# Performance work log

Measured on AMD Instinct MI355X. Metric: run time of the kernel, lower is better.

The kernel has to match this reference:

```python
import jax, jax.numpy as jnp
import numpy as np
import math

THETA = 10000.0

def apply_rope(x, start_pos=0):
    # x: [B, H, S, D], rotate-half RoPE
    B, H, S, D = x.shape
    pos = jnp.arange(start_pos, start_pos + S, dtype=jnp.float32)
    inv_freq = 1.0 / (THETA ** (jnp.arange(0, D, 2, dtype=jnp.float32) / D))  # [D/2]
    ang = pos[:, None] * inv_freq[None, :]  # [S, D/2]
    cos, sin = jnp.cos(ang), jnp.sin(ang)
    x1, x2 = jnp.split(x, 2, axis=-1)
    return jnp.concatenate([x1 * cos - x2 * sin, x1 * sin + x2 * cos], axis=-1)


def setup_inputs() -> dict:
    key = jax.random.key(0)
    ks = jax.random.split(key, 9)
    B, S, E, H, D = 2, 2048, 2048, 16, 128
    s = 0.02
    return {
        "x": jax.random.normal(ks[0], (B, S, E), jnp.float32),
        "W_q": jax.random.normal(ks[1], (E, H * D), jnp.float32) * s,
        "b_q": jnp.zeros((H * D,), jnp.float32),
        "W_k": jax.random.normal(ks[2], (E, D), jnp.float32) * s,
        "b_k": jnp.zeros((D,), jnp.float32),
        "W_v": jax.random.normal(ks[3], (E, D), jnp.float32) * s,
        "b_v": jnp.zeros((D,), jnp.float32),
        "W_o": jax.random.normal(ks[4], (H * D, E), jnp.float32) * s,
        "b_o": jnp.zeros((E,), jnp.float32),
    }


def reference(x, W_q, b_q, W_k, b_k, W_v, b_v, W_o, b_o):
    B, S, E = x.shape
    D = W_k.shape[1]
    H = W_q.shape[1] // D
    # projections (weights stored [in, out])
    q = (x @ W_q + b_q).reshape(B, S, H, D).transpose(0, 2, 1, 3)   # [B,H,S,D]
    k = (x @ W_k + b_k).reshape(B, S, 1, D).transpose(0, 2, 1, 3)   # [B,1,S,D]
    v = (x @ W_v + b_v).reshape(B, S, 1, D).transpose(0, 2, 1, 3)   # [B,1,S,D]
    # RoPE (cache is None -> start_pos = 0)
    q = apply_rope(q, 0)
    k = apply_rope(k, 0)
    # shared-KV attention: k head dim broadcasts over H q heads
    scores = jnp.einsum("bhqd,bokd->bhqk", q, k) / math.sqrt(D)     # [B,H,S,S]
    causal = jnp.tril(jnp.ones((S, S), dtype=bool))
    scores = jnp.where(causal, scores, -jnp.inf)
    attn = jax.nn.softmax(scores, axis=-1)
    out = jnp.einsum("bhqk,bokd->bhqd", attn, v)                    # [B,H,S,D]
    out = out.transpose(0, 2, 1, 3).reshape(B, S, H * D)
    out = out @ W_o + b_o                                           # dropout is identity in eval
    return out
```

## Files before the change

### kernel.cpp

```cpp
#include <hip/hip_runtime.h>
#include <stdint.h>

typedef __bf16 bf16x8 __attribute__((ext_vector_type(8)));
typedef __bf16 bf16x2 __attribute__((ext_vector_type(2)));
typedef float  f32x4  __attribute__((ext_vector_type(4)));
typedef short  s16x8  __attribute__((ext_vector_type(8)));

__device__ inline unsigned short f2b(float f) {
  unsigned int u = __builtin_bit_cast(unsigned int, f);
  u += 0x7FFFu + ((u >> 16) & 1u);
  return (unsigned short)(u >> 16);
}
__device__ inline float b2f(unsigned short h) {
  unsigned int u = ((unsigned int)h) << 16;
  return __builtin_bit_cast(float, u);
}
__device__ inline unsigned int pkcvt(float a, float b) {
  bf16x2 t;
  t[0] = (__bf16)a;
  t[1] = (__bf16)b;
  return __builtin_bit_cast(unsigned int, t);
}
__device__ inline void gload_lds16(const void* g, void* l) {
  __builtin_amdgcn_global_load_lds(
      (const __attribute__((address_space(1))) unsigned int*)g,
      (__attribute__((address_space(3))) unsigned int*)l, 16, 0, 0);
}

__global__ void k_cvt_bf16(const float* __restrict__ in, unsigned short* __restrict__ out, int n4) {
  int i = blockIdx.x * blockDim.x + threadIdx.x;
  if (i < n4) {
    float4 v = ((const float4*)in)[i];
    ushort4 o;
    o.x = f2b(v.x); o.y = f2b(v.y); o.z = f2b(v.z); o.w = f2b(v.w);
    ((ushort4*)out)[i] = o;
  }
}

__global__ void k_transpose(const float* __restrict__ Wq, const float* __restrict__ Wk,
                            const float* __restrict__ Wv, const float* __restrict__ Wo,
                            unsigned short* __restrict__ dstQKV, unsigned short* __restrict__ dstO) {
  __shared__ float tile[32][33];
  int n0 = blockIdx.x * 32;
  int k0 = blockIdx.y * 32;
  const float* src; int ldn, noff, K;
  unsigned short* dst;
  if (blockIdx.z == 0) {
    K = 2048; dst = dstQKV;
    if (n0 < 2048)       { src = Wq; ldn = 2048; noff = n0; }
    else if (n0 < 2176)  { src = Wk; ldn = 128;  noff = n0 - 2048; }
    else                 { src = Wv; ldn = 128;  noff = n0 - 2176; }
  } else {
    if (n0 >= 2048) return;
    K = 2048; dst = dstO;
    src = Wo; ldn = 2048; noff = n0;
  }
  int tx = threadIdx.x & 31, ty = threadIdx.x >> 5;
  for (int yy = ty; yy < 32; yy += 8)
    tile[yy][tx] = src[(size_t)(k0 + yy) * ldn + noff + tx];
  __syncthreads();
  for (int yy = ty; yy < 32; yy += 8)
    dst[(size_t)(n0 + yy) * K + k0 + tx] = f2b(tile[tx][yy]);
}

template<int BIAS3>
__global__ __launch_bounds__(256)
void k_gemm96(const unsigned short* __restrict__ A, const unsigned short* __restrict__ Bt,
              const float* __restrict__ b0, const float* __restrict__ b1,
              const float* __restrict__ b2, unsigned short* __restrict__ Cout,
              int M, int N, int K) {
  __shared__ unsigned short As[3][4096];
  __shared__ unsigned short Bs[3][3072];
  const int tid  = threadIdx.x;
  const int lane = tid & 63, wid = tid >> 6;
  const int lr = lane & 15, lk = lane >> 4;
  const int wr = wid >> 1,  wc = wid & 1;

  const int nwg = gridDim.x * gridDim.y;
  const int flat = blockIdx.y * gridDim.x + blockIdx.x;
  const int swz = (flat & 7) * (nwg >> 3) + (flat >> 3);
  const int mb = (swz / gridDim.x) * 128;
  const int nb = (swz % gridDim.x) * 96;

  const int srow = tid >> 2, scb = (tid & 3) * 8;
  const size_t gA = (size_t)(mb + srow) * K + scb;
  const int brow0 = wid * 32 + (lane >> 2);
  const int bcol  = (lane & 3) * 8;
  const size_t gB = (size_t)(nb + brow0) * K + bcol;
  const int bdst0 = (wid * 128 + lane) * 16;

  f32x4 acc[4][3];
  #pragma unroll
  for (int i = 0; i < 4; ++i)
    #pragma unroll
    for (int j = 0; j < 3; ++j) acc[i][j] = (f32x4){0.f, 0.f, 0.f, 0.f};

  auto stage = [&](int buf, int kt) {
    const size_t ko = (size_t)kt * 32;
    gload_lds16(A + gA + ko,                  &As[buf][(tid) * 8]);
    gload_lds16(A + gA + 64 * (size_t)K + ko, &As[buf][2048 + tid * 8]);
    if (wid < 3) {
      gload_lds16(Bt + gB + ko,                  (char*)&Bs[buf][0] + bdst0);
      gload_lds16(Bt + gB + 16 * (size_t)K + ko, (char*)&Bs[buf][0] + bdst0 + 1024);
    }
  };

  const int ktn = K >> 5;
  stage(0, 0);
  stage(1, 1);

  int cur = 0;
  #pragma unroll 1
  for (int kt = 0; kt < ktn; ++kt) {
    if (kt + 2 < ktn) {
      int nbuf = cur + 2; if (nbuf >= 3) nbuf -= 3;
      stage(nbuf, kt + 2);
      if (wid < 3) asm volatile("s_waitcnt vmcnt(8)" ::: "memory");
      else         asm volatile("s_waitcnt vmcnt(4)" ::: "memory");
    } else if (kt + 1 < ktn) {
      if (wid < 3) asm volatile("s_waitcnt vmcnt(4)" ::: "memory");
      else         asm volatile("s_waitcnt vmcnt(2)" ::: "memory");
    } else {
      asm volatile("s_waitcnt vmcnt(0)" ::: "memory");
    }
    __builtin_amdgcn_sched_barrier(0);
    __builtin_amdgcn_s_barrier();
    bf16x8 af[4], bfv[3];
    #pragma unroll
    for (int m = 0; m < 4; ++m)
      af[m]  = *(const bf16x8*)&As[cur][(wr * 64 + m * 16 + lr) * 32 + lk * 8];
    #pragma unroll
    for (int n = 0; n < 3; ++n)
      bfv[n] = *(const bf16x8*)&Bs[cur][(wc * 48 + n * 16 + lr) * 32 + lk * 8];
    #pragma unroll
    for (int m = 0; m < 4; ++m)
      #pragma unroll
      for (int n = 0; n < 3; ++n)
        acc[m][n] = __builtin_amdgcn_mfma_f32_16x16x32_bf16(af[m], bfv[n], acc[m][n], 0, 0, 0);
    __builtin_amdgcn_s_barrier();
    ++cur; if (cur == 3) cur = 0;
  }

  const int r0 = mb + wr * 64, c0 = nb + wc * 48;
  #pragma unroll
  for (int m = 0; m < 4; ++m) {
    #pragma unroll
    for (int n = 0; n < 3; ++n) {
      int col = c0 + n * 16 + lr;
      float bb;
      if (BIAS3) bb = (col < 2048) ? b0[col] : (col < 2176 ? b1[col - 2048] : b2[col - 2176]);
      else       bb = b0[col];
      #pragma unroll
      for (int r = 0; r < 4; ++r) {
        int row = r0 + m * 16 + lk * 4 + r;
        Cout[(size_t)row * N + col] = f2b(acc[m][n][r] + bb);
      }
    }
  }
}

template<int OUT_BF16, int BIAS3>
__global__ __launch_bounds__(256)
void k_gemm_lds(const unsigned short* __restrict__ A, const unsigned short* __restrict__ Bt,
                const float* __restrict__ b0, const float* __restrict__ b1,
                const float* __restrict__ b2, void* __restrict__ Cout,
                int M, int N, int K) {
  __shared__ unsigned short As[3][4096];
  __shared__ unsigned short Bs[3][4096];
  const int tid  = threadIdx.x;
  const int lane = tid & 63, wid = tid >> 6;
  const int lr = lane & 15, lk = lane >> 4;
  const int wr = wid >> 1,  wc = wid & 1;

  const int nwg = gridDim.x * gridDim.y;
  const int flat = blockIdx.y * gridDim.x + blockIdx.x;
  const int swz = (flat & 7) * (nwg >> 3) + (flat >> 3);
  const int mb = (swz / gridDim.x) * 128;
  const int nb = (swz % gridDim.x) * 128;

  const int srow = tid >> 2, scb = (tid & 3) * 8;
  const size_t gA = (size_t)(mb + srow) * K + scb;
  const size_t gB = (size_t)(nb + srow) * K + scb;
  const int ldso = wid * 512;

  f32x4 acc[4][4];
  #pragma unroll
  for (int i = 0; i < 4; ++i)
    #pragma unroll
    for (int j = 0; j < 4; ++j) acc[i][j] = (f32x4){0.f, 0.f, 0.f, 0.f};

  auto stage = [&](int buf, int kt) {
    const size_t ko = (size_t)kt * 32;
    gload_lds16(A  + gA + ko,                  &As[buf][ldso]);
    gload_lds16(A  + gA + 64 * (size_t)K + ko, &As[buf][2048 + ldso]);
    gload_lds16(Bt + gB + ko,                  &Bs[buf][ldso]);
    gload_lds16(Bt + gB + 64 * (size_t)K + ko, &Bs[buf][2048 + ldso]);
  };

  const int ktn = K >> 5;
  stage(0, 0);
  stage(1, 1);

  int cur = 0;
  #pragma unroll 1
  for (int kt = 0; kt < ktn; ++kt) {
    if (kt + 2 < ktn) {
      int nbuf = cur + 2; if (nbuf >= 3) nbuf -= 3;
      stage(nbuf, kt + 2);
      asm volatile("s_waitcnt vmcnt(8)" ::: "memory");
    } else if (kt + 1 < ktn) {
      asm volatile("s_waitcnt vmcnt(4)" ::: "memory");
    } else {
      asm volatile("s_waitcnt vmcnt(0)" ::: "memory");
    }
    __builtin_amdgcn_sched_barrier(0);
    __builtin_amdgcn_s_barrier();
    bf16x8 af[4], bfv[4];
    #pragma unroll
    for (int m = 0; m < 4; ++m)
      af[m]  = *(const bf16x8*)&As[cur][(wr * 64 + m * 16 + lr) * 32 + lk * 8];
    #pragma unroll
    for (int n = 0; n < 4; ++n)
      bfv[n] = *(const bf16x8*)&Bs[cur][(wc * 64 + n * 16 + lr) * 32 + lk * 8];
    #pragma unroll
    for (int m = 0; m < 4; ++m)
      #pragma unroll
      for (int n = 0; n < 4; ++n)
        acc[m][n] = __builtin_amdgcn_mfma_f32_16x16x32_bf16(af[m], bfv[n], acc[m][n], 0, 0, 0);
    __builtin_amdgcn_s_barrier();
    ++cur; if (cur == 3) cur = 0;
  }

  const int r0 = mb + wr * 64, c0 = nb + wc * 64;
  #pragma unroll
  for (int m = 0; m < 4; ++m) {
    #pragma unroll
    for (int n = 0; n < 4; ++n) {
      int col = c0 + n * 16 + lr;
      float bb;
      if (BIAS3) bb = (col < 2048) ? b0[col] : (col < 2176 ? b1[col - 2048] : b2[col - 2176]);
      else       bb = b0[col];
      #pragma unroll
      for (int r = 0; r < 4; ++r) {
        int row = r0 + m * 16 + lk * 4 + r;
        float v = acc[m][n][r] + bb;
        if (OUT_BF16) ((unsigned short*)Cout)[(size_t)row * N + col] = f2b(v);
        else          ((float*)Cout)[(size_t)row * N + col] = v;
      }
    }
  }
}

__global__ void k_rope(const unsigned short* __restrict__ qkv,
                       unsigned short* __restrict__ qr,
                       unsigned short* __restrict__ kr,
                       int S, int H) {
  int R = blockIdx.x * 4 + (threadIdx.x >> 6);
  int lane = threadIdx.x & 63;
  int per_b = S * (H + 1);
  int b = R / per_b;
  int rem = R - b * per_b;
  int s = rem / (H + 1);
  int j = rem - s * (H + 1);
  const unsigned short* src = qkv + (size_t)(b * S + s) * 2304 + (j < H ? j * 128 : 2048);
  float x1 = b2f(src[lane]);
  float x2 = b2f(src[lane + 64]);
  float invf = expf(-(float)lane * (9.210340371976184f / 64.0f));
  float ang = (float)s * invf;
  float c = cosf(ang), sn = sinf(ang);
  float o1 = x1 * c - x2 * sn;
  float o2 = x1 * sn + x2 * c;
  unsigned short* dst;
  if (j < H) {
    const float scale = 0.08838834764831845f;
    o1 *= scale; o2 *= scale;
    dst = qr + ((size_t)(b * H + j) * S + s) * 128;
  } else {
    dst = kr + ((size_t)(b * S) + s) * 128;
  }
  dst[lane]      = f2b(o1);
  dst[lane + 64] = f2b(o2);
}

__global__ void k_vtrans(const unsigned short* __restrict__ qkv,
                         unsigned short* __restrict__ vt, int S) {
  __shared__ unsigned short tile[32][33];
  int b = blockIdx.z;
  int s0 = blockIdx.x * 32, d0 = blockIdx.y * 32;
  int tx = threadIdx.x & 31, ty = threadIdx.x >> 5;
  for (int yy = ty; yy < 32; yy += 8)
    tile[yy][tx] = qkv[(size_t)(b * S + s0 + yy) * 2304 + 2176 + d0 + tx];
  __syncthreads();
  for (int yy = ty; yy < 32; yy += 8)
    vt[((size_t)b * 128 + d0 + yy) * S + s0 + tx] = tile[tx][yy];
}

__global__ __launch_bounds__(256, 2)
void k_attn(const unsigned short* __restrict__ qr,
            const unsigned short* __restrict__ kr,
            const unsigned short* __restrict__ vt,
            unsigned short* __restrict__ attn_out,
            unsigned short* __restrict__ pscr,
            float* __restrict__ lscr,
            int S, int H) {
  const int flat = blockIdx.x + 16 * blockIdx.y + 256 * blockIdx.z;
  const int half = flat >> 8;
  const int p    = flat & 7;
  const int h    = (flat >> 3) & 15;
  const int b    = (flat >> 7) & 1;
  const int qtA = 8 + p, qtB = 7 - p;
  const int qb0A = qtA * 128, qb0B = qtB * 128;
  const int nA = 2 * qtA + 2;
  const int pg = (b * H + h) * 8 + p;

  const int tid = threadIdx.x, wid = tid >> 6, lane = tid & 63;
  const int lr = lane & 15, lk = lane >> 4;

  __shared__ unsigned short Kt[2][64 * 128];
  __shared__ unsigned short Vt[2][128 * 64];

  const char* kbyte = (const char*)(kr + (size_t)b * S * 128);
  const char* vbyte = (const char*)(vt + (size_t)b * 128 * S);
  const size_t vrow_bytes = (size_t)S * 2;

  bf16x8 aq[2][4];
  auto loadQ = [&](int qb0) {
    #pragma unroll
    for (int g = 0; g < 2; ++g) {
      const unsigned short* qptr = qr + ((size_t)(b * H + h) * S + (qb0 + wid * 32 + g * 16 + lr)) * 128;
      #pragma unroll
      for (int kk = 0; kk < 4; ++kk) aq[g][kk] = *(const bf16x8*)(qptr + kk * 32 + lk * 8);
    }
  };

  f32x4 acc[2][8];
  float ls[2];
  auto resetAcc = [&]() {
    #pragma unroll
    for (int g = 0; g < 2; ++g) {
      ls[g] = 0.f;
      #pragma unroll
      for (int t = 0; t < 8; ++t) acc[g][t] = (f32x4){0.f, 0.f, 0.f, 0.f};
    }
  };

  const int vsw = ((lr & 3) | ((lr >> 1) & 4)) << 4;
  int krow_[4], ksw_[4];
  #pragma unroll
  for (int m = 0; m < 4; ++m) {
    int row = ((m >> 1) << 5) + ((m & 1) << 2) + ((lr >> 2) << 3) + (lr & 3);
    krow_[m] = row;
    ksw_[m] = ((row & 3) | ((row >> 1) & 4)) << 4;
  }

  auto stage = [&](int buf, int kb) {
    const char* kg = kbyte + (size_t)kb * 256;
    #pragma unroll
    for (int r = 0; r < 4; ++r) {
      int row = (tid >> 4) + r * 16;
      int sw = ((row & 3) | ((row >> 1) & 4)) << 4;
      const char* src = kg + row * 256 + (((tid & 15) << 4) ^ sw);
      gload_lds16(src, (void*)((char*)&Kt[buf][0] + r * 4096 + wid * 1024));
    }
    const char* vg = vbyte + (size_t)kb * 2;
    #pragma unroll
    for (int r = 0; r < 4; ++r) {
      int d = (tid >> 3) + r * 32;
      int sw = ((d & 3) | ((d >> 1) & 4)) << 4;
      const char* src = vg + (size_t)d * vrow_bytes + (((tid & 7) << 4) ^ sw);
      gload_lds16(src, (void*)((char*)&Vt[buf][0] + r * 4096 + wid * 1024));
    }
  };

  auto itemKb = [&](int j, int& which) -> int {
    int idx = half * 17 + j;
    if (idx < nA) { which = 0; return idx * 64; }
    which = 1; return (idx - nA) * 64;
  };

  auto flushA = [&]() {
    #pragma unroll
    for (int g = 0; g < 2; ++g) {
      float v = ls[g];
      v += __shfl_xor(v, 16);
      v += __shfl_xor(v, 32);
      if (lk == 0) lscr[((size_t)pg * 2 + half) * 128 + wid * 32 + g * 16 + lr] = v;
      #pragma unroll
      for (int t = 0; t < 8; ++t)
        #pragma unroll
        for (int r = 0; r < 4; ++r) {
          int row = wid * 32 + g * 16 + lk * 4 + r;
          pscr[((size_t)pg * 2 + half) * 16384 + row * 128 + t * 16 + lr] = f2b(acc[g][t][r]);
        }
    }
  };

  auto computeTile = [&](int cur, int kb, int qb0cur) {
    const int qw = qb0cur + wid * 32;
    if (kb > qw + 31) return;
    const unsigned short* Kc = &Kt[cur][0];
    const unsigned short* Vc = &Vt[cur][0];
    f32x4 s4[2][4];
    #pragma unroll
    for (int g = 0; g < 2; ++g)
      #pragma unroll
      for (int m = 0; m < 4; ++m) s4[g][m] = (f32x4){0.f, 0.f, 0.f, 0.f};
    __builtin_amdgcn_s_setprio(1);
    #pragma unroll
    for (int kk = 0; kk < 4; ++kk) {
      bf16x8 kfk[4];
      #pragma unroll
      for (int m = 0; m < 4; ++m)
        kfk[m] = *(const bf16x8*)((const char*)Kc + krow_[m] * 256 + ((kk * 64 + lk * 16) ^ ksw_[m]));
      #pragma unroll
      for (int m = 0; m < 4; ++m) {
        s4[0][m] = __builtin_amdgcn_mfma_f32_16x16x32_bf16(kfk[m], aq[0][kk], s4[0][m], 0, 0, 0);
        s4[1][m] = __builtin_amdgcn_mfma_f32_16x16x32_bf16(kfk[m], aq[1][kk], s4[1][m], 0, 0, 0);
      }
    }
    __builtin_amdgcn_s_setprio(0);
    bf16x8 pa[2][2];
    #pragma unroll
    for (int g = 0; g < 2; ++g) {
      const int rowq = qw + g * 16 + lr;
      const bool domask = (kb + 64) > (qw + g * 16);
      uint2 pk[4];
      #pragma unroll
      for (int m = 0; m < 4; ++m) {
        const int kb_m = kb + ((m >> 1) << 5) + ((m & 1) << 2) + lk * 8;
        float pv[4];
        #pragma unroll
        for (int r = 0; r < 4; ++r) {
          float v = __expf(s4[g][m][r]);
          if (domask && (kb_m + r) > rowq) v = 0.f;
          pv[r] = v;
          ls[g] += v;
        }
        pk[m].x = pkcvt(pv[0], pv[1]);
        pk[m].y = pkcvt(pv[2], pv[3]);
      }
      uint4 ua, ub;
      ua.x = pk[0].x; ua.y = pk[0].y; ua.z = pk[1].x; ua.w = pk[1].y;
      ub.x = pk[2].x; ub.y = pk[2].y; ub.z = pk[3].x; ub.w = pk[3].y;
      pa[g][0] = __builtin_bit_cast(bf16x8, ua);
      pa[g][1] = __builtin_bit_cast(bf16x8, ub);
    }
    __builtin_amdgcn_s_setprio(1);
    #pragma unroll
    for (int t = 0; t < 8; ++t) {
      const char* vl = (const char*)(Vc + (t * 16 + lr) * 64);
      bf16x8 bv0 = *(const bf16x8*)(vl + ((lk * 16) ^ vsw));
      bf16x8 bv1 = *(const bf16x8*)(vl + ((64 + lk * 16) ^ vsw));
      acc[0][t] = __builtin_amdgcn_mfma_f32_16x16x32_bf16(pa[0][0], bv0, acc[0][t], 0, 0, 0);
      acc[1][t] = __builtin_amdgcn_mfma_f32_16x16x32_bf16(pa[1][0], bv0, acc[1][t], 0, 0, 0);
      acc[0][t] = __builtin_amdgcn_mfma_f32_16x16x32_bf16(pa[0][1], bv1, acc[0][t], 0, 0, 0);
      acc[1][t] = __builtin_amdgcn_mfma_f32_16x16x32_bf16(pa[1][1], bv1, acc[1][t], 0, 0, 0);
    }
    __builtin_amdgcn_s_setprio(0);
  };

  loadQ(qb0A);
  resetAcc();
  int curTile = 0, qb0cur = qb0A;

  {
    int wh0;
    stage(0, itemKb(0, wh0));
  }
  int cur = 0;
  #pragma unroll 1
  for (int j = 0; j < 17; ++j) {
    if (j + 1 < 17) {
      int whn;
      stage(cur ^ 1, itemKb(j + 1, whn));
      asm volatile("s_waitcnt vmcnt(8)" ::: "memory");
    } else {
      asm volatile("s_waitcnt vmcnt(0)" ::: "memory");
    }
    __builtin_amdgcn_sched_barrier(0);
    __builtin_amdgcn_s_barrier();
    int wh;
    const int kb = itemKb(j, wh);
    if (wh != curTile) {
      flushA();
      resetAcc();
      loadQ(qb0B);
      curTile = 1;
      qb0cur = qb0B;
    }
    computeTile(cur, kb, qb0cur);
    __builtin_amdgcn_s_barrier();
    cur ^= 1;
  }

  if (half == 0) {
    flushA();
  } else {
    #pragma unroll
    for (int g = 0; g < 2; ++g) {
      float v = ls[g];
      v += __shfl_xor(v, 16);
      v += __shfl_xor(v, 32);
      float rl[4];
      #pragma unroll
      for (int r = 0; r < 4; ++r) rl[r] = 1.0f / __shfl(v, lk * 4 + r);
      #pragma unroll
      for (int t = 0; t < 8; ++t) {
        #pragma unroll
        for (int r = 0; r < 4; ++r) {
          int srow = qb0B + wid * 32 + g * 16 + lk * 4 + r;
          float o = acc[g][t][r] * rl[r];
          attn_out[((size_t)(b * S) + srow) * 2048 + h * 128 + t * 16 + lr] = f2b(o);
        }
      }
    }
  }
}

__global__ void k_combine(const unsigned short* __restrict__ pscr,
                          const float* __restrict__ lscr,
                          unsigned short* __restrict__ attn_out, int S, int H) {
  const int p = blockIdx.x, h = blockIdx.y, b = blockIdx.z;
  const int pg = (b * H + h) * 8 + p;
  const int qb0A = (8 + p) * 128;
  const int tid = threadIdx.x;
  const unsigned short* p0 = pscr + (size_t)pg * 2 * 16384;
  const unsigned short* p1 = p0 + 16384;
  const float* l0 = lscr + (size_t)pg * 2 * 128;
  const float* l1 = l0 + 128;
  #pragma unroll
  for (int it = 0; it < 8; ++it) {
    int row = it * 16 + (tid >> 4);
    int col = (tid & 15) * 8;
    float rl = 1.0f / (l0[row] + l1[row]);
    ushort4 a = *(const ushort4*)(p0 + row * 128 + col);
    ushort4 c = *(const ushort4*)(p1 + row * 128 + col);
    ushort4 a2 = *(const ushort4*)(p0 + row * 128 + col + 4);
    ushort4 c2 = *(const ushort4*)(p1 + row * 128 + col + 4);
    ushort4 o1, o2;
    o1.x = f2b((b2f(a.x) + b2f(c.x)) * rl);
    o1.y = f2b((b2f(a.y) + b2f(c.y)) * rl);
    o1.z = f2b((b2f(a.z) + b2f(c.z)) * rl);
    o1.w = f2b((b2f(a.w) + b2f(c.w)) * rl);
    o2.x = f2b((b2f(a2.x) + b2f(c2.x)) * rl);
    o2.y = f2b((b2f(a2.y) + b2f(c2.y)) * rl);
    o2.z = f2b((b2f(a2.z) + b2f(c2.z)) * rl);
    o2.w = f2b((b2f(a2.w) + b2f(c2.w)) * rl);
    unsigned short* dst = attn_out + ((size_t)(b * S) + qb0A + row) * 2048 + h * 128 + col;
    *(ushort4*)dst = o1;
    *(ushort4*)(dst + 4) = o2;
  }
}

extern "C" void kernel_launch(void* const* d_in, const int* in_sizes, int n_in,
                              void* d_out, int out_size, void* d_ws, size_t ws_size,
                              hipStream_t stream) {
  const float* x  = (const float*)d_in[0];
  const float* Wq = (const float*)d_in[1];
  const float* bq = (const float*)d_in[2];
  const float* Wk = (const float*)d_in[3];
  const float* bk = (const float*)d_in[4];
  const float* Wv = (const float*)d_in[5];
  const float* bv = (const float*)d_in[6];
  const float* Wo = (const float*)d_in[7];
  const float* bo = (const float*)d_in[8];

  const int B = 2, S = 2048, E = 2048, H = 16, D = 128;
  const int M = B * S;
  const int Nqkv = H * D + 2 * D;

  char* w = (char*)d_ws;
  unsigned short* xb    = (unsigned short*)w;
  unsigned short* WqkvT = (unsigned short*)(w + 16777216);
  unsigned short* qkv   = (unsigned short*)(w + 16777216 + 9437184);
  unsigned short* qr    = (unsigned short*)(w + 16777216 + 9437184 + 18874368);
  unsigned short* kr    = qr + (size_t)B * H * S * D;
  unsigned short* vtb   = kr + (size_t)B * S * D;
  float*          cbias = (float*)(vtb + (size_t)B * S * D);
  unsigned short* WoT   = (unsigned short*)(cbias + 4096);
  unsigned short* attn_out = xb;
  unsigned short* pscr  = qkv;
  float*          lscr  = (float*)WqkvT;

  k_cvt_bf16<<<dim3((M * E / 4) / 256), 256, 0, stream>>>(x, xb, M * E / 4);
  k_transpose<<<dim3(Nqkv / 32, E / 32, 2), 256, 0, stream>>>(Wq, Wk, Wv, Wo, WqkvT, WoT);
  k_gemm96<1><<<dim3(Nqkv / 96, M / 128), 256, 0, stream>>>(xb, WqkvT, bq, bk, bv, qkv, M, Nqkv, E);
  k_rope<<<dim3(B * S * (H + 1) / 4), 256, 0, stream>>>(qkv, qr, kr, S, H);
  k_vtrans<<<dim3(S / 32, D / 32, B), 256, 0, stream>>>(qkv, vtb, S);
  k_attn<<<dim3(16, 16, 2), 256, 0, stream>>>(qr, kr, vtb, attn_out, pscr, lscr, S, H);
  k_combine<<<dim3(8, H, B), 256, 0, stream>>>(pscr, lscr, attn_out, S, H);
  k_gemm_lds<0, 0><<<dim3(E / 128, M / 128), 256, 0, stream>>>(attn_out, WoT, bo, nullptr, nullptr, (void*)d_out, M, E, H * D);
}
```

Baseline: 195.5 us.

## Fuse x fp32-to-bf16 conversion into QKV GEMM A-load, double-buffer GEMMs

Removes the separate kernel that converted x to bf16. The QKV GEMM now reads fp32 x through registers, converts it, and writes it to LDS while B still streams via global_load_lds. That GEMM moves from a 96-wide to a 128-wide N tile (2304/128 = 18 columns), and both GEMMs go from triple to double buffering. This saves a kernel launch plus an extra write and read of the bf16 copy of x. In exchange the A path now goes through registers and VALU, and the shallower pipeline may hide latency less well.

```diff
diff --git a/kernel.cpp b/kernel.cpp
--- a/kernel.cpp
+++ b/kernel.cpp
@@ -4,7 +4,6 @@
 typedef __bf16 bf16x8 __attribute__((ext_vector_type(8)));
 typedef __bf16 bf16x2 __attribute__((ext_vector_type(2)));
 typedef float  f32x4  __attribute__((ext_vector_type(4)));
-typedef short  s16x8  __attribute__((ext_vector_type(8)));
 
 __device__ inline unsigned short f2b(float f) {
   unsigned int u = __builtin_bit_cast(unsigned int, f);
@@ -25,16 +24,6 @@
   __builtin_amdgcn_global_load_lds(
       (const __attribute__((address_space(1))) unsigned int*)g,
       (__attribute__((address_space(3))) unsigned int*)l, 16, 0, 0);
-}
-
-__global__ void k_cvt_bf16(const float* __restrict__ in, unsigned short* __restrict__ out, int n4) {
-  int i = blockIdx.x * blockDim.x + threadIdx.x;
-  if (i < n4) {
-    float4 v = ((const float4*)in)[i];
-    ushort4 o;
-    o.x = f2b(v.x); o.y = f2b(v.y); o.z = f2b(v.z); o.w = f2b(v.w);
-    ((ushort4*)out)[i] = o;
-  }
 }
 
 __global__ void k_transpose(const float* __restrict__ Wq, const float* __restrict__ Wk,
@@ -63,14 +52,13 @@
     dst[(size_t)(n0 + yy) * K + k0 + tx] = f2b(tile[tx][yy]);
 }
 
-template<int BIAS3>
 __global__ __launch_bounds__(256)
-void k_gemm96(const unsigned short* __restrict__ A, const unsigned short* __restrict__ Bt,
-              const float* __restrict__ b0, const float* __restrict__ b1,
-              const float* __restrict__ b2, unsigned short* __restrict__ Cout,
-              int M, int N, int K) {
-  __shared__ unsigned short As[3][4096];
-  __shared__ unsigned short Bs[3][3072];
+void k_gemmA(const float* __restrict__ A, const unsigned short* __restrict__ Bt,
+             const float* __restrict__ b0, const float* __restrict__ b1,
+             const float* __restrict__ b2, unsigned short* __restrict__ Cout,
+             int M, int N, int K) {
+  __shared__ unsigned short As[2][4096];
+  __shared__ unsigned short Bs[2][4096];
   const int tid  = threadIdx.x;
   const int lane = tid & 63, wid = tid >> 6;
   const int lr = lane & 15, lk = lane >> 4;
@@ -80,76 +68,86 @@
   const int flat = blockIdx.y * gridDim.x + blockIdx.x;
   const int swz = (flat & 7) * (nwg >> 3) + (flat >> 3);
   const int mb = (swz / gridDim.x) * 128;
-  const int nb = (swz % gridDim.x) * 96;
-
-  const int srow = tid >> 2, scb = (tid & 3) * 8;
-  const size_t gA = (size_t)(mb + srow) * K + scb;
-  const int brow0 = wid * 32 + (lane >> 2);
-  const int bcol  = (lane & 3) * 8;
-  const size_t gB = (size_t)(nb + brow0) * K + bcol;
-  const int bdst0 = (wid * 128 + lane) * 16;
-
-  f32x4 acc[4][3];
+  const int nb = (swz % gridDim.x) * 128;
+
+  const int srow = tid >> 2, sc8 = (tid & 3) * 8;
+  const float* gA0 = A + (size_t)(mb + srow) * K + sc8;
+  const float* gA1 = A + (size_t)(mb + srow + 64) * K + sc8;
+  const size_t gB = (size_t)(nb + srow) * K + sc8;
+  const int ldso = wid * 512;
+  const int awo = srow * 32 + sc8;
+
+  f32x4 acc[4][4];
   #pragma unroll
   for (int i = 0; i < 4; ++i)
     #pragma unroll
-    for (int j = 0; j < 3; ++j) acc[i][j] = (f32x4){0.f, 0.f, 0.f, 0.f};
-
-  auto stage = [&](int buf, int kt) {
+    for (int j = 0; j < 4; ++j) acc[i][j] = (f32x4){0.f, 0.f, 0.f, 0.f};
+
+  float4 ap[4];
+  auto loadA = [&](int kt) {
+    const float* p0 = gA0 + kt * 32;
+    const float* p1 = gA1 + kt * 32;
+    ap[0] = *(const float4*)p0;  ap[1] = *(const float4*)(p0 + 4);
+    ap[2] = *(const float4*)p1;  ap[3] = *(const float4*)(p1 + 4);
+  };
+  auto writeA = [&](int buf) {
+    uint4 w0, w1;
+    w0.x = pkcvt(ap[0].x, ap[0].y); w0.y = pkcvt(ap[0].z, ap[0].w);
+    w0.z = pkcvt(ap[1].x, ap[1].y); w0.w = pkcvt(ap[1].z, ap[1].w);
+    w1.x = pkcvt(ap[2].x, ap[2].y); w1.y = pkcvt(ap[2].z, ap[2].w);
+    w1.z = pkcvt(ap[3].x, ap[3].y); w1.w = pkcvt(ap[3].z, ap[3].w);
+    *(uint4*)&As[buf][awo]        = w0;
+    *(uint4*)&As[buf][2048 + awo] = w1;
+  };
+  auto stageB = [&](int buf, int kt) {
     const size_t ko = (size_t)kt * 32;
-    gload_lds16(A + gA + ko,                  &As[buf][(tid) * 8]);
-    gload_lds16(A + gA + 64 * (size_t)K + ko, &As[buf][2048 + tid * 8]);
-    if (wid < 3) {
-      gload_lds16(Bt + gB + ko,                  (char*)&Bs[buf][0] + bdst0);
-      gload_lds16(Bt + gB + 16 * (size_t)K + ko, (char*)&Bs[buf][0] + bdst0 + 1024);
-    }
+    gload_lds16(Bt + gB + ko,                  &Bs[buf][ldso]);
+    gload_lds16(Bt + gB + 64 * (size_t)K + ko, &Bs[buf][2048 + ldso]);
   };
 
   const int ktn = K >> 5;
-  stage(0, 0);
-  stage(1, 1);
+  loadA(0); stageB(0, 0);
+  writeA(0);
+  if (ktn > 1) { loadA(1); stageB(1, 1); }
+  asm volatile("s_waitcnt vmcnt(%0) lgkmcnt(0)" :: "i"(6) : "memory");
+  __builtin_amdgcn_sched_barrier(0);
 
   int cur = 0;
   #pragma unroll 1
   for (int kt = 0; kt < ktn; ++kt) {
-    if (kt + 2 < ktn) {
-      int nbuf = cur + 2; if (nbuf >= 3) nbuf -= 3;
-      stage(nbuf, kt + 2);
-      if (wid < 3) asm volatile("s_waitcnt vmcnt(8)" ::: "memory");
-      else         asm volatile("s_waitcnt vmcnt(4)" ::: "memory");
-    } else if (kt + 1 < ktn) {
-      if (wid < 3) asm volatile("s_waitcnt vmcnt(4)" ::: "memory");
-      else         asm volatile("s_waitcnt vmcnt(2)" ::: "memory");
-    } else {
-      asm volatile("s_waitcnt vmcnt(0)" ::: "memory");
-    }
-    __builtin_amdgcn_sched_barrier(0);
     __builtin_amdgcn_s_barrier();
-    bf16x8 af[4], bfv[3];
+    bf16x8 af[4], bfv[4];
     #pragma unroll
     for (int m = 0; m < 4; ++m)
       af[m]  = *(const bf16x8*)&As[cur][(wr * 64 + m * 16 + lr) * 32 + lk * 8];
     #pragma unroll
-    for (int n = 0; n < 3; ++n)
-      bfv[n] = *(const bf16x8*)&Bs[cur][(wc * 48 + n * 16 + lr) * 32 + lk * 8];
+    for (int n = 0; n < 4; ++n)
+      bfv[n] = *(const bf16x8*)&Bs[cur][(wc * 64 + n * 16 + lr) * 32 + lk * 8];
     #pragma unroll
     for (int m = 0; m < 4; ++m)
       #pragma unroll
-      for (int n = 0; n < 3; ++n)
+      for (int n = 0; n < 4; ++n)
         acc[m][n] = __builtin_amdgcn_mfma_f32_16x16x32_bf16(af[m], bfv[n], acc[m][n], 0, 0, 0);
+    if (kt + 1 < ktn) writeA(cur ^ 1);
     __builtin_amdgcn_s_barrier();
-    ++cur; if (cur == 3) cur = 0;
-  }
-
-  const int r0 = mb + wr * 64, c0 = nb + wc * 48;
+    if (kt + 2 < ktn) {
+      loadA(kt + 2);
+      stageB(cur, kt + 2);
+      asm volatile("s_waitcnt vmcnt(6) lgkmcnt(0)" ::: "memory");
+    } else {
+      asm volatile("s_waitcnt vmcnt(0) lgkmcnt(0)" ::: "memory");
+    }
+    __builtin_amdgcn_sched_barrier(0);
+    cur ^= 1;
+  }
+
+  const int r0 = mb + wr * 64, c0 = nb + wc * 64;
   #pragma unroll
   for (int m = 0; m < 4; ++m) {
     #pragma unroll
-    for (int n = 0; n < 3; ++n) {
+    for (int n = 0; n < 4; ++n) {
       int col = c0 + n * 16 + lr;
-      float bb;
-      if (BIAS3) bb = (col < 2048) ? b0[col] : (col < 2176 ? b1[col - 2048] : b2[col - 2176]);
-      else       bb = b0[col];
+      float bb = (col < 2048) ? b0[col] : (col < 2176 ? b1[col - 2048] : b2[col - 2176]);
       #pragma unroll
       for (int r = 0; r < 4; ++r) {
         int row = r0 + m * 16 + lk * 4 + r;
@@ -159,14 +157,12 @@
   }
 }
 
-template<int OUT_BF16, int BIAS3>
 __global__ __launch_bounds__(256)
-void k_gemm_lds(const unsigned short* __restrict__ A, const unsigned short* __restrict__ Bt,
-                const float* __restrict__ b0, const float* __restrict__ b1,
-                const float* __restrict__ b2, void* __restrict__ Cout,
-                int M, int N, int K) {
-  __shared__ unsigned short As[3][4096];
-  __shared__ unsigned short Bs[3][4096];
+void k_gemm2(const unsigned short* __restrict__ A, const unsigned short* __restrict__ Bt,
+             const float* __restrict__ b0, float* __restrict__ Cout,
+             int M, int N, int K) {
+  __shared__ unsigned short As[2][4096];
+  __shared__ unsigned short Bs[2][4096];
   const int tid  = threadIdx.x;
   const int lane = tid & 63, wid = tid >> 6;
   const int lr = lane & 15, lk = lane >> 4;
@@ -199,16 +195,12 @@
 
   const int ktn = K >> 5;
   stage(0, 0);
-  stage(1, 1);
 
   int cur = 0;
   #pragma unroll 1
   for (int kt = 0; kt < ktn; ++kt) {
-    if (kt + 2 < ktn) {
-      int nbuf = cur + 2; if (nbuf >= 3) nbuf -= 3;
-      stage(nbuf, kt + 2);
-      asm volatile("s_waitcnt vmcnt(8)" ::: "memory");
-    } else if (kt + 1 < ktn) {
+    if (kt + 1 < ktn) {
+      stage(cur ^ 1, kt + 1);
       asm volatile("s_waitcnt vmcnt(4)" ::: "memory");
     } else {
       asm volatile("s_waitcnt vmcnt(0)" ::: "memory");
@@ -228,7 +220,7 @@
       for (int n = 0; n < 4; ++n)
         acc[m][n] = __builtin_amdgcn_mfma_f32_16x16x32_bf16(af[m], bfv[n], acc[m][n], 0, 0, 0);
     __builtin_amdgcn_s_barrier();
-    ++cur; if (cur == 3) cur = 0;
+    cur ^= 1;
   }
 
   const int r0 = mb + wr * 64, c0 = nb + wc * 64;
@@ -237,15 +229,11 @@
     #pragma unroll
     for (int n = 0; n < 4; ++n) {
       int col = c0 + n * 16 + lr;
-      float bb;
-      if (BIAS3) bb = (col < 2048) ? b0[col] : (col < 2176 ? b1[col - 2048] : b2[col - 2176]);
-      else       bb = b0[col];
+      float bb = b0[col];
       #pragma unroll
       for (int r = 0; r < 4; ++r) {
         int row = r0 + m * 16 + lk * 4 + r;
-        float v = acc[m][n][r] + bb;
-        if (OUT_BF16) ((unsigned short*)Cout)[(size_t)row * N + col] = f2b(v);
-        else          ((float*)Cout)[(size_t)row * N + col] = v;
+        Cout[(size_t)row * N + col] = acc[m][n][r] + bb;
       }
     }
   }
@@ -570,7 +558,7 @@
   const int Nqkv = H * D + 2 * D;
 
   char* w = (char*)d_ws;
-  unsigned short* xb    = (unsigned short*)w;
+  unsigned short* attn_out = (unsigned short*)w;
   unsigned short* WqkvT = (unsigned short*)(w + 16777216);
   unsigned short* qkv   = (unsigned short*)(w + 16777216 + 9437184);
   unsigned short* qr    = (unsigned short*)(w + 16777216 + 9437184 + 18874368);
@@ -578,16 +566,14 @@
   unsigned short* vtb   = kr + (size_t)B * S * D;
   float*          cbias = (float*)(vtb + (size_t)B * S * D);
   unsigned short* WoT   = (unsigned short*)(cbias + 4096);
-  unsigned short* attn_out = xb;
   unsigned short* pscr  = qkv;
   float*          lscr  = (float*)WqkvT;
 
-  k_cvt_bf16<<<dim3((M * E / 4) / 256), 256, 0, stream>>>(x, xb, M * E / 4);
   k_transpose<<<dim3(Nqkv / 32, E / 32, 2), 256, 0, stream>>>(Wq, Wk, Wv, Wo, WqkvT, WoT);
-  k_gemm96<1><<<dim3(Nqkv / 96, M / 128), 256, 0, stream>>>(xb, WqkvT, bq, bk, bv, qkv, M, Nqkv, E);
+  k_gemmA<<<dim3(Nqkv / 128, M / 128), 256, 0, stream>>>(x, WqkvT, bq, bk, bv, qkv, M, Nqkv, E);
   k_rope<<<dim3(B * S * (H + 1) / 4), 256, 0, stream>>>(qkv, qr, kr, S, H);
   k_vtrans<<<dim3(S / 32, D / 32, B), 256, 0, stream>>>(qkv, vtb, S);
   k_attn<<<dim3(16, 16, 2), 256, 0, stream>>>(qr, kr, vtb, attn_out, pscr, lscr, S, H);
   k_combine<<<dim3(8, H, B), 256, 0, stream>>>(pscr, lscr, attn_out, S, H);
-  k_gemm_lds<0, 0><<<dim3(E / 128, M / 128), 256, 0, stream>>>(attn_out, WoT, bo, nullptr, nullptr, (void*)d_out, M, E, H * D);
-}
+  k_gemm2<<<dim3(E / 128, M / 128), 256, 0, stream>>>(attn_out, WoT, bo, (float*)d_out, M, E, H * D);
+}
```

Result: slower. 215.8 us (+10.4%).
